# Kernel tuning notes

Measured on AMD Instinct MI355X. Metric: run time of the kernel, lower is better.

## Reference

```python
import jax, jax.numpy as jnp
import numpy as np

ORDER = 64
DT = 1.0 / 2048.0
L, BATCH, SIZE = 2048, 8, 64


def _hippo_legt(N):
    # HiPPO-LegT (LMU) continuous-time transition, as in s4 repo transition()
    Q = np.arange(N, dtype=np.float64)
    R = (2 * Q + 1) ** 0.5
    j, i = np.meshgrid(Q, Q)
    A = R[:, None] * np.where(i < j, (-1.0) ** (i - j), 1.0) * R[None, :]
    B = R[:, None]
    return -A, B


def _bilinear_discretize(A, B, dt):
    # scipy.signal.cont2discrete(..., method='bilinear')
    N = A.shape[0]
    I = np.eye(N)
    M = np.linalg.inv(I - (dt / 2.0) * A)
    Ad = M @ (I + (dt / 2.0) * A)
    Bd = M @ (dt * B)
    return Ad, Bd


def setup_inputs() -> dict:
    key = jax.random.key(0)
    inputs = jax.random.normal(key, (L, BATCH, SIZE), dtype=jnp.float32)
    Ac, Bc = _hippo_legt(ORDER)
    Ad, Bd = _bilinear_discretize(Ac, Bc, DT)
    return {
        "inputs": inputs,
        "A": jnp.asarray(Ad, dtype=jnp.float32),   # (order, order) discrete transition
        "Bm": jnp.asarray(Bd, dtype=jnp.float32),  # (order, 1) discrete input matrix
    }


def reference(inputs, A, Bm):
    # inputs: (L, B, S); A: (N, N); Bm: (N, 1)
    # u = F.linear(inputs.unsqueeze(-1), Bm): u[l,b,s,n] = inputs[l,b,s] * Bm[n,0]
    u = inputs[..., None] * Bm[:, 0]  # (L, B, S, N)

    # parallel_unroll_recursive computes x_t = A x_{t-1} + u_t with x_{-1} = 0
    def step(x, u_t):
        x_new = jnp.einsum('nm,bsm->bsn', A, x) + u_t
        return x_new, x_new

    x0 = jnp.zeros((inputs.shape[1], inputs.shape[2], A.shape[0]), dtype=inputs.dtype)
    _, out = jax.lax.scan(step, x0, u)
    return out  # (L, B, S, N)
```

## Files before the change

kernel.cpp:

```cpp
#include <hip/hip_runtime.h>


typedef _Float16 f16;
typedef __attribute__((ext_vector_type(8))) _Float16 f16x8;
typedef __attribute__((ext_vector_type(4))) float f32x4;

__global__ __launch_bounds__(1024) void kA_pow(
    const float* __restrict__ A, const float* __restrict__ Bm,
    float* __restrict__ A64, float* __restrict__ Kv, f16* __restrict__ W16)
{
  __shared__ __align__(16) f16 Ah[64][72],  Al[64][72];
  __shared__ __align__(16) f16 B0h[64][72], B0l[64][72];
  __shared__ __align__(16) f16 B1h[64][72], B1l[64][72];
  __shared__ __align__(16) f16 Y8h[64][72], Y8l[64][72];
  __shared__ __align__(16) f16 Ybh[64][72], Ybl[64][72];

  int tau = blockIdx.x;
  int e = tau + 1;
  int a = e >> 3, b = e & 7;
  int t = threadIdx.x;
  int wave = t >> 6, lane = t & 63;
  int tn = wave >> 2, tm = wave & 3;
  int kg = lane >> 4, fr = lane & 15;

  auto mm = [&](f16 (*Ph)[72], f16 (*Pl)[72], f16 (*Qh)[72], f16 (*Ql)[72],
                f16 (*Dh)[72], f16 (*Dl)[72]) {
    f32x4 acc = {};
    #pragma unroll
    for (int kk = 0; kk < 2; ++kk) {
      f16x8 ah = *(const f16x8*)&Ph[tn * 16 + fr][kk * 32 + kg * 8];
      f16x8 al = *(const f16x8*)&Pl[tn * 16 + fr][kk * 32 + kg * 8];
      f16x8 bh = *(const f16x8*)&Qh[tm * 16 + fr][kk * 32 + kg * 8];
      f16x8 bl = *(const f16x8*)&Ql[tm * 16 + fr][kk * 32 + kg * 8];
      acc = __builtin_amdgcn_mfma_f32_16x16x32_f16(ah, bh, acc, 0, 0, 0);
      acc = __builtin_amdgcn_mfma_f32_16x16x32_f16(ah, bl, acc, 0, 0, 0);
      acc = __builtin_amdgcn_mfma_f32_16x16x32_f16(al, bh, acc, 0, 0, 0);
    }
    #pragma unroll
    for (int r = 0; r < 4; ++r) {
      float v = acc[r];
      f16 h = (f16)v, l = (f16)(v - (float)h);
      Dh[tn * 16 + kg * 4 + r][tm * 16 + fr] = h;
      Dl[tn * 16 + kg * 4 + r][tm * 16 + fr] = l;
    }
    __syncthreads();
  };
  auto cpy2 = [&](f16 (*Sh)[72], f16 (*Sl)[72], f16 (*Dh)[72], f16 (*Dl)[72]) {
    const unsigned* sh = (const unsigned*)Sh; unsigned* dh = (unsigned*)Dh;
    const unsigned* sl = (const unsigned*)Sl; unsigned* dl = (unsigned*)Dl;
    for (int idx = t; idx < 2304; idx += 1024) { dh[idx] = sh[idx]; dl[idx] = sl[idx]; }
  };

  for (int idx = t; idx < 4096; idx += 1024) {
    float v = A[idx];
    int r = idx >> 6, c2 = idx & 63;
    f16 h = (f16)v, l = (f16)(v - (float)h);
    Ah[r][c2] = h;  Al[r][c2] = l;
    B0h[c2][r] = h; B0l[c2][r] = l;
  }
  __syncthreads();

  f16 (*curH)[72] = B0h; f16 (*curL)[72] = B0l;
  f16 (*othH)[72] = B1h; f16 (*othL)[72] = B1l;
  auto swp = [&]() {
    f16 (*tH)[72] = curH; curH = othH; othH = tH;
    f16 (*tL)[72] = curL; curL = othL; othL = tL;
  };

  if (b == 1) cpy2(curH, curL, Ybh, Ybl);

  int loMax = (a >= 1) ? 8 : b;
  for (int i = 2; i <= loMax; ++i) {
    mm(curH, curL, Ah, Al, othH, othL);
    swp();
    if (i == b) cpy2(curH, curL, Ybh, Ybl);
    if (i == 8) cpy2(curH, curL, Y8h, Y8l);
  }

  f16 (*Rh)[72]; f16 (*Rl)[72]; bool tr;
  if (a == 0) {
    Rh = curH; Rl = curL; tr = true;
  } else {
    for (int idx = t; idx < 4096; idx += 1024) {
      int i = idx >> 6, j = idx & 63;
      othH[i][j] = curH[j][i];
      othL[i][j] = curL[j][i];
    }
    swp();
    __syncthreads();
    for (int a2 = 2; a2 <= a; ++a2) {
      mm(curH, curL, Y8h, Y8l, othH, othL);
      swp();
    }
    if (b >= 1) {
      mm(curH, curL, Ybh, Ybl, othH, othL);
      swp();
    }
    Rh = curH; Rl = curL; tr = false;
  }

  for (int idx = t; idx < 4096; idx += 1024) {
    int wn = idx >> 6, m = idx & 63;
    f16 h = tr ? Rh[m][wn] : Rh[wn][m];
    f16 l = tr ? Rl[m][wn] : Rl[wn][m];
    f16* wrow = W16 + ((size_t)(tau * 64 + wn)) * 256;
    wrow[64 + m] = h; wrow[128 + m] = l; wrow[192 + m] = h;
    if (tau == 63) A64[idx] = (float)h + (float)l;
  }
  if (t < 64) {
    float s = 0.f;
    #pragma unroll 8
    for (int m = 0; m < 64; ++m) {
      float pv = tr ? ((float)Rh[m][t] + (float)Rl[m][t])
                    : ((float)Rh[t][m] + (float)Rl[t][m]);
      s += pv * Bm[m];
    }
    if (tau < 63) Kv[(tau + 1) * 64 + t] = s;
    else          Kv[t] = Bm[t];
  }
}

__global__ __launch_bounds__(256) void kB_prep(
    const float* __restrict__ inp, const float* __restrict__ Kv,
    const float* __restrict__ A64,
    f16* __restrict__ R16, f16* __restrict__ W16)
{
  __shared__ __align__(16) float sm[64 * 132];
  int t = threadIdx.x;
  int b = blockIdx.x;
  if (b < 128) {
    float (*tile)[132] = (float (*)[132])sm;
    int j = b >> 2, qb = (b & 3) * 128;
    {
      int k = t >> 2, sg = (t & 3) * 32;
      const float* src = inp + j * 32768 + k * 512 + qb + sg;
      #pragma unroll
      for (int i = 0; i < 32; i += 4)
        *(f32x4*)(&tile[k][sg + i]) = *(const f32x4*)(src + i);
    }
    __syncthreads();
    int q = t >> 1, kh = (t & 1) * 32;
    f16 tmp[32];
    #pragma unroll
    for (int kk = 0; kk < 32; ++kk)
      tmp[kk] = (f16)tile[kh + kk][q];
    f16* dst = R16 + ((size_t)(j * 512 + qb + q)) * 256 + kh;
    #pragma unroll
    for (int v = 0; v < 4; ++v)
      *(f16x8*)(dst + v * 8) = *(const f16x8*)(&tmp[v * 8]);
  } else if (b < 192) {
    int tau = b - 128;
    float* KT = sm;
    for (int idx = t; idx < 4096; idx += 256) KT[idx] = Kv[idx];
    __syncthreads();
    int wn = t & 63, kq = t >> 6;
    f16* wrow = W16 + ((size_t)(tau * 64 + wn)) * 256 + kq * 16;
    #pragma unroll
    for (int ki = 0; ki < 16; ++ki) {
      int k = kq * 16 + ki;
      wrow[ki] = (f16)((k <= tau) ? KT[(tau - k) * 64 + wn] : 0.0f);
    }
  } else {
    int wv = t >> 6, L = t & 63;
    int q = (b - 192) * 4 + wv;
    float ar[64], kvr[64];
    #pragma unroll
    for (int m = 0; m < 64; m += 4) {
      f32x4 v4 = *(const f32x4*)(A64 + L * 64 + m);
      ar[m] = v4.x; ar[m + 1] = v4.y; ar[m + 2] = v4.z; ar[m + 3] = v4.w;
    }
    #pragma unroll
    for (int k = 0; k < 64; ++k) kvr[k] = Kv[(63 - k) * 64 + L];
    float x = 0.f;
    float v = inp[(size_t)L * 512 + q];
    for (int j = 0; j < 32; ++j) {
      float vn = (j < 31) ? inp[(size_t)((j + 1) * 64 + L) * 512 + q] : 0.f;
      f16 hh = (f16)x, ll = (f16)(x - (float)hh);
      f16* row = R16 + ((size_t)(j * 512 + q)) * 256;
      row[64 + L] = hh; row[128 + L] = hh; row[192 + L] = ll;
      float a0 = 0.f, a1 = 0.f, c0 = 0.f, c1 = 0.f;
      #pragma unroll
      for (int m = 0; m < 64; m += 2) {
        a0 += ar[m]     * __shfl(x, m);
        a1 += ar[m + 1] * __shfl(x, m + 1);
        c0 += kvr[m]    * __shfl(v, m);
        c1 += kvr[m + 1]* __shfl(v, m + 1);
      }
      x = (a0 + a1) + (c0 + c1);
      v = vn;
    }
  }
}

__global__ __launch_bounds__(256) void kC_gemm(
    const f16* __restrict__ R16, const f16* __restrict__ W16,
    float* __restrict__ out)
{
  __shared__ __align__(16) char smem[2 * 128 * 72 * 2];
  f16 (*Asm)[72] = (f16 (*)[72])smem;
  f16 (*Bsm)[72] = (f16 (*)[72])(smem + 128 * 72 * 2);
  float (*stg)[68] = (float (*)[68])smem;
  int wg = blockIdx.x;
  int swz = (wg & 7) * 512 + (wg >> 3);
  int mt = swz >> 5, nt = swz & 31;
  int t = threadIdx.x, wave = t >> 6, lane = t & 63;
  int wr = wave >> 1, wc = wave & 1;
  int kg = lane >> 4, fr = lane & 15;
  f32x4 acc[4][4] = {};
  f16x8 pa[4], pb[4];

  auto issue = [&](int ks) {
    #pragma unroll
    for (int ii = 0; ii < 4; ++ii) {
      int s = t + ii * 256;
      int row = s >> 3, sg = (s & 7) * 8;
      pa[ii] = *(const f16x8*)(R16 + ((size_t)(mt * 128 + row)) * 256 + ks * 64 + sg);
      pb[ii] = *(const f16x8*)(W16 + ((size_t)(nt * 128 + row)) * 256 + ks * 64 + sg);
    }
  };

  issue(0);
  for (int ks = 0; ks < 4; ++ks) {
    #pragma unroll
    for (int ii = 0; ii < 4; ++ii) {
      int s = t + ii * 256;
      int row = s >> 3, sg = (s & 7) * 8;
      *(f16x8*)(&Asm[row][sg]) = pa[ii];
      *(f16x8*)(&Bsm[row][sg]) = pb[ii];
    }
    if (ks < 3) issue(ks + 1);
    __syncthreads();
    #pragma unroll
    for (int kk = 0; kk < 2; ++kk) {
      f16x8 af[4], bf[4];
      #pragma unroll
      for (int i = 0; i < 4; ++i) {
        af[i] = *(const f16x8*)(&Asm[wr * 64 + i * 16 + fr][kk * 32 + kg * 8]);
        bf[i] = *(const f16x8*)(&Bsm[wc * 64 + i * 16 + fr][kk * 32 + kg * 8]);
      }
      #pragma unroll
      for (int mi = 0; mi < 4; ++mi)
        #pragma unroll
        for (int ni = 0; ni < 4; ++ni)
          acc[mi][ni] = __builtin_amdgcn_mfma_f32_16x16x32_f16(
              af[mi], bf[ni], acc[mi][ni], 0, 0, 0);
    }
    __syncthreads();
  }
  int j = mt >> 2, q0 = (mt & 3) * 128;
  #pragma unroll
  for (int half = 0; half < 2; ++half) {
    if (wc == half) {
      #pragma unroll
      for (int mi = 0; mi < 4; ++mi)
        #pragma unroll
        for (int ni = 0; ni < 4; ++ni)
          #pragma unroll
          for (int r = 0; r < 4; ++r)
            stg[wr * 64 + mi * 16 + kg * 4 + r][ni * 16 + fr] = acc[mi][ni][r];
    }
    __syncthreads();
    int tau_g = nt * 2 + half;
    float* obase = out + (size_t)j * 2097152 + (size_t)tau_g * 32768 + (size_t)q0 * 64;
    #pragma unroll
    for (int it = 0; it < 8; ++it) {
      int fi = it * 1024 + t * 4;
      int rr = fi >> 6, cc = fi & 63;
      __builtin_nontemporal_store(*(const f32x4*)(&stg[rr][cc]),
                                  (f32x4*)(obase + fi));
    }
    __syncthreads();
  }
}

extern "C" void kernel_launch(void* const* d_in, const int* in_sizes, int n_in,
                              void* d_out, int out_size, void* d_ws, size_t ws_size,
                              hipStream_t stream)
{
  (void)in_sizes; (void)n_in; (void)out_size; (void)ws_size;
  const float* inp = (const float*)d_in[0];
  const float* A   = (const float*)d_in[1];
  const float* Bm  = (const float*)d_in[2];
  float* out = (float*)d_out;

  float* ws = (float*)d_ws;
  float* A64 = ws;
  float* Kv  = ws + 4096;
  f16*  W16  = (f16*)(ws + 8192);
  f16*  R16  = (f16*)((char*)d_ws + 2129920);

  hipLaunchKernelGGL(kA_pow,  dim3(64),   dim3(1024), 0, stream, A, Bm, A64, Kv, W16);
  hipLaunchKernelGGL(kB_prep, dim3(320),  dim3(256),  0, stream, inp, Kv, A64, R16, W16);
  hipLaunchKernelGGL(kC_gemm, dim3(4096), dim3(256),  0, stream, R16, W16, out);
}
```

Measured before the change: 124.6 us.

## Load GEMM fragments directly from global memory, drop shared-memory staging

The GEMM kernel now reads MFMA operand fragments straight from global memory into registers with a two-deep register double buffer, removing the LDS staging of A and B tiles and the barriers around each k-step. Shared memory is kept only for the output staging tile, and launch bounds request 3 blocks per SIMD. This cuts LDS traffic and synchronisation, but global loads become less coalesced (16-byte strided rows) and each element is reloaded by two waves, relying on caches.

```diff
diff --git a/kernel.cpp b/kernel.cpp
--- a/kernel.cpp
+++ b/kernel.cpp
@@ -192,64 +192,53 @@
   }
 }
 
-__global__ __launch_bounds__(256) void kC_gemm(
+__global__ __launch_bounds__(256, 3) void kC_gemm(
     const f16* __restrict__ R16, const f16* __restrict__ W16,
     float* __restrict__ out)
 {
-  __shared__ __align__(16) char smem[2 * 128 * 72 * 2];
-  f16 (*Asm)[72] = (f16 (*)[72])smem;
-  f16 (*Bsm)[72] = (f16 (*)[72])(smem + 128 * 72 * 2);
-  float (*stg)[68] = (float (*)[68])smem;
+  __shared__ __align__(16) float stg[128][68];
   int wg = blockIdx.x;
   int swz = (wg & 7) * 512 + (wg >> 3);
   int mt = swz >> 5, nt = swz & 31;
   int t = threadIdx.x, wave = t >> 6, lane = t & 63;
   int wr = wave >> 1, wc = wave & 1;
   int kg = lane >> 4, fr = lane & 15;
+
+  const f16* Abase = R16 + ((size_t)(mt * 128 + wr * 64 + fr)) * 256 + kg * 8;
+  const f16* Bbase = W16 + ((size_t)(nt * 128 + wc * 64 + fr)) * 256 + kg * 8;
+
   f32x4 acc[4][4] = {};
-  f16x8 pa[4], pb[4];
-
-  auto issue = [&](int ks) {
-    #pragma unroll
-    for (int ii = 0; ii < 4; ++ii) {
-      int s = t + ii * 256;
-      int row = s >> 3, sg = (s & 7) * 8;
-      pa[ii] = *(const f16x8*)(R16 + ((size_t)(mt * 128 + row)) * 256 + ks * 64 + sg);
-      pb[ii] = *(const f16x8*)(W16 + ((size_t)(nt * 128 + row)) * 256 + ks * 64 + sg);
-    }
-  };
-
-  issue(0);
-  for (int ks = 0; ks < 4; ++ks) {
-    #pragma unroll
-    for (int ii = 0; ii < 4; ++ii) {
-      int s = t + ii * 256;
-      int row = s >> 3, sg = (s & 7) * 8;
-      *(f16x8*)(&Asm[row][sg]) = pa[ii];
-      *(f16x8*)(&Bsm[row][sg]) = pb[ii];
-    }
-    if (ks < 3) issue(ks + 1);
-    __syncthreads();
-    #pragma unroll
-    for (int kk = 0; kk < 2; ++kk) {
-      f16x8 af[4], bf[4];
-      #pragma unroll
-      for (int i = 0; i < 4; ++i) {
-        af[i] = *(const f16x8*)(&Asm[wr * 64 + i * 16 + fr][kk * 32 + kg * 8]);
-        bf[i] = *(const f16x8*)(&Bsm[wc * 64 + i * 16 + fr][kk * 32 + kg * 8]);
-      }
-      #pragma unroll
-      for (int mi = 0; mi < 4; ++mi)
-        #pragma unroll
-        for (int ni = 0; ni < 4; ++ni)
-          acc[mi][ni] = __builtin_amdgcn_mfma_f32_16x16x32_f16(
-              af[mi], bf[ni], acc[mi][ni], 0, 0, 0);
-    }
-    __syncthreads();
-  }
+  f16x8 aC[4], bC[4], aN[4], bN[4];
+
+  auto LD = [&](int g, f16x8* av, f16x8* bv) {
+    #pragma unroll
+    for (int i = 0; i < 4; ++i) {
+      av[i] = *(const f16x8*)(Abase + i * 16 * 256 + g * 32);
+      bv[i] = *(const f16x8*)(Bbase + i * 16 * 256 + g * 32);
+    }
+  };
+  auto MM = [&](const f16x8* av, const f16x8* bv) {
+    #pragma unroll
+    for (int mi = 0; mi < 4; ++mi)
+      #pragma unroll
+      for (int ni = 0; ni < 4; ++ni)
+        acc[mi][ni] = __builtin_amdgcn_mfma_f32_16x16x32_f16(
+            av[mi], bv[ni], acc[mi][ni], 0, 0, 0);
+  };
+
+  LD(0, aC, bC);
+  #pragma unroll
+  for (int h = 0; h < 4; ++h) {
+    LD(2 * h + 1, aN, bN);
+    MM(aC, bC);
+    if (h < 3) LD(2 * h + 2, aC, bC);
+    MM(aN, bN);
+  }
+
   int j = mt >> 2, q0 = (mt & 3) * 128;
   #pragma unroll
   for (int half = 0; half < 2; ++half) {
+    __syncthreads();
     if (wc == half) {
       #pragma unroll
       for (int mi = 0; mi < 4; ++mi)
@@ -269,7 +258,6 @@
       __builtin_nontemporal_store(*(const f32x4*)(&stg[rr][cc]),
                                   (f32x4*)(obase + fi));
     }
-    __syncthreads();
   }
 }
 
```

Result: slower. 220.8 us (+77.2%).
